# Performance work log

Measured on AMD Instinct MI355X. Metric: run time of the kernel, lower is better.

Reference implementation:

```python
import jax, jax.numpy as jnp
from jax import lax
import numpy as np

B, T = 256, 100
N_FEAT, V, E, H = 64, 32, 8, 512
CAT_POS = np.arange(0, N_FEAT, 4)                                 # 16 categorical feature indices
CONT_POS = np.array([k for k in range(N_FEAT) if k % 4 != 0])      # 48 continuous feature indices
N_CAT, N_CONT = len(CAT_POS), len(CONT_POS)
IN_LEN = N_FEAT + N_CAT * (E - 1)                                  # 176, matches input_linear.in_features
N_LAYERS = 2                                                        # len(hidden_layers) - 1 LSTMs

# Precompute the interleaved output layout of embed(): walking feature index k,
# categorical features occupy E slots, continuous features 1 slot.
def _layout():
    cont_off, cat_off, cur = [], [], 0
    for k in range(N_FEAT):
        if k % 4 == 0:
            cat_off.append(cur); cur += E
        else:
            cont_off.append(cur); cur += 1
    return np.array(cont_off), np.array(cat_off)
CONT_OFF, CAT_OFF = _layout()
CAT_COLS = (CAT_OFF[:, None] + np.arange(E)).ravel()               # [N_CAT*E] target columns


def lstm(x, Wih, Whh, bih, bhh):
    # PyTorch LSTM, batch_first, gate order (i, f, g, o).
    xw = jnp.einsum('bti,gi->btg', x, Wih) + bih                   # [B,T,4H] input projection (one GEMM)
    def step(carry, xw_t):
        h, c = carry
        gates = xw_t + h @ Whh.T + bhh
        i, f, g, o = jnp.split(gates, 4, axis=-1)
        c = jax.nn.sigmoid(f) * c + jax.nn.sigmoid(i) * jnp.tanh(g)
        h = jax.nn.sigmoid(o) * jnp.tanh(c)
        return (h, c), h
    h0 = jnp.zeros((x.shape[0], Whh.shape[1]), x.dtype)
    (_, _), hs = lax.scan(step, (h0, h0), jnp.swapaxes(xw, 0, 1))
    return jnp.swapaxes(hs, 0, 1)                                   # [B,T,H]


def setup_inputs() -> dict:
    key = jax.random.key(0)
    ks = jax.random.split(key, 16)
    s = 0.05
    base = jax.random.normal(ks[0], (B, T, N_FEAT), jnp.float32)
    cats = jax.random.randint(ks[1], (B, T, N_CAT), 0, V)
    x = base.at[..., CAT_POS].set(cats.astype(jnp.float32))
    return {
        'x': x,
        'scaler_mean': jax.random.normal(ks[2], (N_FEAT,), jnp.float32),
        'scaler_scale': jax.random.uniform(ks[3], (N_FEAT,), jnp.float32, minval=0.5, maxval=2.0),
        'emb': jax.random.normal(ks[4], (N_CAT, V, E), jnp.float32) * s,
        'W_in': jax.random.normal(ks[5], (IN_LEN, H), jnp.float32) * s,
        'b_in': jnp.zeros((H,), jnp.float32),
        'Wih': jax.random.normal(ks[6], (N_LAYERS, 4 * H, H), jnp.float32) * s,
        'Whh': jax.random.normal(ks[7], (N_LAYERS, 4 * H, H), jnp.float32) * s,
        'bih': jnp.zeros((N_LAYERS, 4 * H), jnp.float32),
        'bhh': jnp.zeros((N_LAYERS, 4 * H), jnp.float32),
        'W_out': jax.random.normal(ks[8], (H, N_CONT), jnp.float32) * s,
        'b_out': jnp.zeros((N_CONT,), jnp.float32),
        'W_cls': jax.random.normal(ks[9], (N_CAT, H, V), jnp.float32) * s,
        'b_cls': jnp.zeros((N_CAT, V), jnp.float32),
    }


def reference(x, scaler_mean, scaler_scale, emb, W_in, b_in, Wih, Whh, bih, bhh, W_out, b_out, W_cls, b_cls):
    # ---- embed(): vectorized replacement of the triple python loop ----
    scaled = (x - scaler_mean) / scaler_scale                      # sklearn StandardScaler.transform
    cont_vals = scaled[..., CONT_POS]                              # [B,T,48]
    idx = x[..., CAT_POS].astype(jnp.int32)                        # [B,T,16] categorical codes
    embv = emb[jnp.arange(N_CAT)[None, None, :], idx]              # [B,T,16,E] gather
    new = jnp.zeros((x.shape[0], x.shape[1], IN_LEN), x.dtype)
    new = new.at[..., CONT_OFF].set(cont_vals)
    new = new.at[..., CAT_COLS].set(embv.reshape(x.shape[0], x.shape[1], N_CAT * E))
    # ---- input linear + activation ----
    h = jax.nn.relu(new @ W_in + b_in)                             # [B,T,512]
    # ---- stacked LSTMs, activation after each ----
    for l in range(N_LAYERS):
        h = jax.nn.relu(lstm(h, Wih[l], Whh[l], bih[l], bhh[l]))
    last = h[:, -1, :]                                             # [B,512]
    cont_out = last @ W_out + b_out                                # [B,48]
    cls_out = jnp.einsum('bh,nhv->bnv', last, W_cls) + b_cls       # [B,16,32] classification heads
    return (cont_out, cls_out)
```

## Files before the change

kernel.cpp:

```cpp
#include <hip/hip_runtime.h>

#define BB 256
#define TT 100
#define HH 512
#define G4 2048
#define INL 176
#define KIN 192
#define NCAT 16
#define NCONT 48
#define VV 32
#define EE 8
#define MTOT (BB*TT)
#define GRPB 32
#define FS 16

typedef unsigned short u16;
typedef unsigned int   u32;
typedef unsigned long long u64;
typedef __attribute__((ext_vector_type(8))) short bf16x8;
typedef __attribute__((ext_vector_type(4))) float f32x4;

__device__ __forceinline__ float bf2f(u16 u){
    union { u32 i; float f; } v; v.i = ((u32)u) << 16; return v.f;
}
__device__ __forceinline__ u16 f2bf(float f){
    union { float f; u32 i; } v; v.f = f;
    u32 b = v.i;
    b += 0x7FFFu + ((b >> 16) & 1u);
    return (u16)(b >> 16);
}
__device__ __forceinline__ float fast_tanh(float x){
    float e = __expf(2.f * x);
    return 1.f - 2.f / (e + 1.f);
}
__device__ __forceinline__ u64 relu4_bf16(u64 v){
    u64 s = v & 0x8000800080008000ULL;
    u64 m = s - (s >> 15);
    return v & ~(s | m);
}

__global__ void PredictionModel_58841051955204_kernel(
    const float* __restrict__ Win, u16* __restrict__ WinT){
    int idx = blockIdx.x*256 + threadIdx.x;
    if (idx >= HH*KIN) return;
    int h = idx / KIN, i = idx % KIN;
    WinT[idx] = (i < INL) ? f2bf(Win[i*HH + h]) : (u16)0;
}

__global__ void k_cvt(const float* __restrict__ in, u16* __restrict__ out, int n){
    int i = blockIdx.x*256 + threadIdx.x;
    if (i < n) out[i] = f2bf(in[i]);
}

__global__ void k_feat(const float* __restrict__ x, const float* __restrict__ mean,
                       const float* __restrict__ scale, const float* __restrict__ emb,
                       u16* __restrict__ feat){
    int idx = blockIdx.x*256 + threadIdx.x;
    int bt = idx >> 4, g = idx & 15;
    if (bt >= MTOT) return;
    const float* xr = x + (size_t)bt*64;
    u16* fr = feat + (size_t)bt*KIN;
    int k0 = g*4;
    int ci = (int)xr[k0];
    if (ci < 0) ci = 0;
    if (ci > VV-1) ci = VV-1;
    const float* ep = emb + (size_t)(g*VV + ci)*EE;
    int c0 = g*11;
    for (int e = 0; e < 8; e++) fr[c0+e] = f2bf(ep[e]);
    for (int j = 1; j <= 3; j++){
        int k = k0 + j;
        fr[c0 + 8 + (j-1)] = f2bf((xr[k] - mean[k]) / scale[k]);
    }
    fr[INL + g] = 0;
}

__global__ __launch_bounds__(256) void k_gemm(
    const u16* __restrict__ A, int lda,
    const u16* __restrict__ W, int K,
    const float* __restrict__ bias1, const float* __restrict__ bias2,
    void* __restrict__ out, int ldo, int kc_cnt, int do_relu, int out_half)
{
    __shared__ u16 sA[64*40];
    __shared__ u16 sB[256*40];
    int tid = threadIdx.x;
    int w = tid >> 6, lane = tid & 63, q = lane >> 4, r = lane & 15;
    int m0 = blockIdx.x * 64;
    int n0 = blockIdx.y * 256;

    f32x4 acc[4][4];
    for (int a_ = 0; a_ < 4; a_++)
        for (int b_ = 0; b_ < 4; b_++){
            acc[a_][b_][0] = 0.f; acc[a_][b_][1] = 0.f;
            acc[a_][b_][2] = 0.f; acc[a_][b_][3] = 0.f;
        }

    for (int kc = 0; kc < kc_cnt; kc++){
        {
            int row = tid >> 2, seg = tid & 3;
            uint4 v = *(const uint4*)(A + (size_t)(m0+row)*lda + kc*32 + seg*8);
            *(uint4*)(&sA[row*40 + seg*8]) = v;
            const u16* wr = W + (size_t)(n0 + tid)*K + kc*32;
            uint4 b0 = *(const uint4*)(wr);
            uint4 b1 = *(const uint4*)(wr+8);
            uint4 b2 = *(const uint4*)(wr+16);
            uint4 b3 = *(const uint4*)(wr+24);
            u16* d = &sB[tid*40];
            *(uint4*)(d)    = b0; *(uint4*)(d+8)  = b1;
            *(uint4*)(d+16) = b2; *(uint4*)(d+24) = b3;
        }
        __syncthreads();
        bf16x8 a[4], b[4];
        for (int mt = 0; mt < 4; mt++) a[mt] = *(const bf16x8*)(&sA[(mt*16 + r)*40 + q*8]);
        for (int i = 0; i < 4; i++)    b[i]  = *(const bf16x8*)(&sB[((w*4+i)*16 + r)*40 + q*8]);
        for (int mt = 0; mt < 4; mt++)
            for (int i = 0; i < 4; i++)
                acc[mt][i] = __builtin_amdgcn_mfma_f32_16x16x32_bf16(a[mt], b[i], acc[mt][i], 0, 0, 0);
        __syncthreads();
    }

    for (int i = 0; i < 4; i++){
        int n = n0 + (w*4+i)*16 + r;
        float bs = 0.f;
        if (bias1) bs += bias1[n];
        if (bias2) bs += bias2[n];
        for (int mt = 0; mt < 4; mt++){
            for (int reg = 0; reg < 4; reg++){
                int m = m0 + mt*16 + q*4 + reg;
                float v = acc[mt][i][reg] + bs;
                if (do_relu) v = fmaxf(v, 0.f);
                if (out_half) ((_Float16*)out)[(size_t)m*ldo + n] = (_Float16)v;
                else          ((u16*)out)[(size_t)m*ldo + n] = f2bf(v);
            }
        }
    }
}

__global__ void k_zcnt(int* bar){
    int i = blockIdx.x*256 + threadIdx.x;
    if (i < 4096)
        __hip_atomic_store(&bar[i], 0, __ATOMIC_RELAXED, __HIP_MEMORY_SCOPE_AGENT);
}

__global__ __launch_bounds__(256, 1) void k_rec2(
    const u16* __restrict__ Wihb,
    const u16* __restrict__ Whhb,
    const u16* __restrict__ Xbuf,
    const float* __restrict__ bih, const float* __restrict__ bhh,
    u64* __restrict__ h0r,
    u64* __restrict__ h1A, u64* __restrict__ h1B,
    int* __restrict__ bar)
{
    extern __shared__ u16 smem[];
    int tid = threadIdx.x;
    int w = tid >> 6, lane = tid & 63, q = lane >> 4, r = lane & 15;
    int lay  = blockIdx.x >> 7;
    int bid7 = blockIdx.x & 127;
    int mg = bid7 & 3, jb = bid7 >> 2;
    int m0 = mg*64, j0 = jb*16;
    int j = j0 + r;
    int* F0x = bar;
    int* F1x = bar + 2048;
    int fidx = (mg*GRPB + jb)*FS;
    const u16* sWih = smem;
    const u16* sWhh = smem + 64*512;

    {
        int row = tid >> 2, seg = tid & 3;
        int g = row >> 4, jj = row & 15;
        const u16* srcI = Wihb + (size_t)lay*G4*HH + (size_t)(g*HH + j0 + jj)*HH;
        const u16* srcW = Whhb + (size_t)lay*G4*HH + (size_t)(g*HH + j0 + jj)*HH;
        for (int i = 0; i < 16; i++){
            int c = seg*16 + i;
            *(uint4*)(&smem[row*512 + ((c ^ (row & 7)) * 8)]) = *(const uint4*)(srcI + c*8);
            *(uint4*)(&smem[64*512 + row*512 + ((c ^ (row & 7)) * 8)]) = *(const uint4*)(srcW + c*8);
        }
    }
    float creg[4] = {0.f, 0.f, 0.f, 0.f};
    if ((r & 3) == 0){
        u64* hz = lay ? h1A : (h0r + (size_t)3*BB*(HH/4));
        for (int reg = 0; reg < 4; reg++){
            int m = m0 + w*16 + q*4 + reg;
            __hip_atomic_store(&hz[(size_t)m*(HH/4) + ((j0 + r) >> 2)], 0ULL,
                               __ATOMIC_RELAXED, __HIP_MEMORY_SCOPE_AGENT);
        }
    }
    asm volatile("s_waitcnt vmcnt(0)" ::: "memory");
    __syncthreads();
    if (tid == 0)
        __hip_atomic_store(lay ? &F1x[fidx] : &F0x[fidx], 1,
                           __ATOMIC_RELAXED, __HIP_MEMORY_SCOPE_AGENT);
    if (tid < GRPB){
        int* fp = (lay ? F1x : F0x) + (mg*GRPB + tid)*FS;
        long long t0c = clock64();
        while (__hip_atomic_load(fp, __ATOMIC_RELAXED, __HIP_MEMORY_SCOPE_AGENT) < 1){
            __builtin_amdgcn_s_sleep(1);
            if (clock64() - t0c > 50000000LL) break;
        }
    }
    __syncthreads();

    float bs[4];
    for (int g = 0; g < 4; g++)
        bs[g] = bih[lay*G4 + g*HH + j] + bhh[lay*G4 + g*HH + j];

    if (!lay){
        const u64* xb = (const u64*)Xbuf;
        u64 xn[32];
        {
            const u64* xrow = xb + ((size_t)(m0 + w*16 + r)*TT + 0)*(HH/4);
            #pragma unroll
            for (int kc = 0; kc < 16; kc++){
                int jg0 = kc*8 + q*2;
                xn[kc*2]   = __builtin_nontemporal_load(&xrow[jg0]);
                xn[kc*2+1] = __builtin_nontemporal_load(&xrow[jg0+1]);
            }
        }

        for (int t = 0; t < TT; t++){
            const u64* hsrc = h0r + (size_t)((t + 3) & 3)*BB*(HH/4);
            u32* hdst32 = (u32*)(h0r + (size_t)(t & 3)*BB*(HH/4));
            const u64* hrow = hsrc + (size_t)(m0 + w*16 + r)*(HH/4);

            u64 hd[32];
            #pragma unroll
            for (int kc = 0; kc < 16; kc++){
                int jg0 = kc*8 + q*2;
                hd[kc*2]   = __hip_atomic_load(&hrow[jg0],   __ATOMIC_RELAXED, __HIP_MEMORY_SCOPE_AGENT);
                hd[kc*2+1] = __hip_atomic_load(&hrow[jg0+1], __ATOMIC_RELAXED, __HIP_MEMORY_SCOPE_AGENT);
            }
            asm volatile("" :
                "+v"(hd[0]),  "+v"(hd[1]),  "+v"(hd[2]),  "+v"(hd[3]),
                "+v"(hd[4]),  "+v"(hd[5]),  "+v"(hd[6]),  "+v"(hd[7]),
                "+v"(hd[8]),  "+v"(hd[9]),  "+v"(hd[10]), "+v"(hd[11]),
                "+v"(hd[12]), "+v"(hd[13]), "+v"(hd[14]), "+v"(hd[15]));
            asm volatile("" :
                "+v"(hd[16]), "+v"(hd[17]), "+v"(hd[18]), "+v"(hd[19]),
                "+v"(hd[20]), "+v"(hd[21]), "+v"(hd[22]), "+v"(hd[23]),
                "+v"(hd[24]), "+v"(hd[25]), "+v"(hd[26]), "+v"(hd[27]),
                "+v"(hd[28]), "+v"(hd[29]), "+v"(hd[30]), "+v"(hd[31]));
            __builtin_amdgcn_sched_barrier(0);

            f32x4 acc[4];
            for (int g = 0; g < 4; g++){
                acc[g][0] = 0.f; acc[g][1] = 0.f; acc[g][2] = 0.f; acc[g][3] = 0.f;
            }
            #pragma unroll
            for (int kc = 0; kc < 16; kc++){
                union { u64 d[2]; bf16x8 v; } au;
                au.d[0] = xn[kc*2];
                au.d[1] = xn[kc*2+1];
                int cbase = kc*4 + q;
                #pragma unroll
                for (int g = 0; g < 4; g++){
                    int row = g*16 + r;
                    bf16x8 b = *(const bf16x8*)(&sWih[row*512 + ((cbase ^ (row & 7)) * 8)]);
                    acc[g] = __builtin_amdgcn_mfma_f32_16x16x32_bf16(au.v, b, acc[g], 0, 0, 0);
                }
            }
            #pragma unroll
            for (int kc = 0; kc < 16; kc++){
                union { u64 d[2]; bf16x8 v; } au;
                au.d[0] = hd[kc*2];
                au.d[1] = hd[kc*2+1];
                int cbase = kc*4 + q;
                #pragma unroll
                for (int g = 0; g < 4; g++){
                    int row = g*16 + r;
                    bf16x8 b = *(const bf16x8*)(&sWhh[row*512 + ((cbase ^ (row & 7)) * 8)]);
                    acc[g] = __builtin_amdgcn_mfma_f32_16x16x32_bf16(au.v, b, acc[g], 0, 0, 0);
                }
            }
            if (t + 1 < TT){
                const u64* xrow = xb + ((size_t)(m0 + w*16 + r)*TT + (t+1))*(HH/4);
                #pragma unroll
                for (int kc = 0; kc < 16; kc++){
                    int jg0 = kc*8 + q*2;
                    xn[kc*2]   = __builtin_nontemporal_load(&xrow[jg0]);
                    xn[kc*2+1] = __builtin_nontemporal_load(&xrow[jg0+1]);
                }
            }

            #pragma unroll
            for (int reg = 0; reg < 4; reg++){
                int m = m0 + w*16 + q*4 + reg;
                float Gi = acc[0][reg] + bs[0];
                float Gf = acc[1][reg] + bs[1];
                float Gg = acc[2][reg] + bs[2];
                float Go = acc[3][reg] + bs[3];
                float iv = 1.f/(1.f + __expf(-Gi));
                float fv = 1.f/(1.f + __expf(-Gf));
                float gv = fast_tanh(Gg);
                float ov = 1.f/(1.f + __expf(-Go));
                float c = fv * creg[reg] + iv * gv;
                creg[reg] = c;
                float h = ov * fast_tanh(c);
                u32 own = (u32)f2bf(h);
                u32 p01 = own | (((u32)__shfl_xor((int)own, 1)) << 16);
                if ((r & 1) == 0){
                    __hip_atomic_store(&hdst32[(size_t)m*(HH/2) + ((j0 + r) >> 1)], p01,
                                       __ATOMIC_RELAXED, __HIP_MEMORY_SCOPE_AGENT);
                }
            }

            asm volatile("s_waitcnt vmcnt(0)" ::: "memory");
            __syncthreads();
            if (tid == 0)
                __hip_atomic_store(&F0x[fidx], t + 2, __ATOMIC_RELAXED, __HIP_MEMORY_SCOPE_AGENT);
            if (t + 1 < TT){
                if (tid < 64){
                    long long t0c = clock64();
                    const int* fp; int thr;
                    if (lane < GRPB){ fp = &F0x[(mg*GRPB + lane)*FS];        thr = t + 2; }
                    else            { fp = &F1x[(mg*GRPB + (lane-GRPB))*FS]; thr = t - 1; }
                    while (__hip_atomic_load(fp, __ATOMIC_RELAXED, __HIP_MEMORY_SCOPE_AGENT) < thr){
                        __builtin_amdgcn_s_sleep(1);
                        if (clock64() - t0c > 50000000LL) break;
                    }
                }
                __syncthreads();
            }
        }
    } else {
        if (tid < GRPB){
            const int* fp = &F0x[(mg*GRPB + tid)*FS];
            long long t0c = clock64();
            while (__hip_atomic_load(fp, __ATOMIC_RELAXED, __HIP_MEMORY_SCOPE_AGENT) < 2){
                __builtin_amdgcn_s_sleep(1);
                if (clock64() - t0c > 50000000LL) break;
            }
        }
        __syncthreads();

        for (int t = 0; t < TT; t++){
            const u64* xsrc = h0r + (size_t)(t & 3)*BB*(HH/4);
            const u64* hsrc = (t & 1) ? h1B : h1A;
            u64*       hdst = (t & 1) ? h1A : h1B;
            const u64* xrow = xsrc + (size_t)(m0 + w*16 + r)*(HH/4);
            const u64* hrow = hsrc + (size_t)(m0 + w*16 + r)*(HH/4);

            u64 hx[32], hh[32];
            #pragma unroll
            for (int kc = 0; kc < 16; kc++){
                int jg0 = kc*8 + q*2;
                hx[kc*2]   = relu4_bf16(__hip_atomic_load(&xrow[jg0],   __ATOMIC_RELAXED, __HIP_MEMORY_SCOPE_AGENT));
                hx[kc*2+1] = relu4_bf16(__hip_atomic_load(&xrow[jg0+1], __ATOMIC_RELAXED, __HIP_MEMORY_SCOPE_AGENT));
            }
            #pragma unroll
            for (int kc = 0; kc < 16; kc++){
                int jg0 = kc*8 + q*2;
                hh[kc*2]   = __hip_atomic_load(&hrow[jg0],   __ATOMIC_RELAXED, __HIP_MEMORY_SCOPE_AGENT);
                hh[kc*2+1] = __hip_atomic_load(&hrow[jg0+1], __ATOMIC_RELAXED, __HIP_MEMORY_SCOPE_AGENT);
            }
            asm volatile("" :
                "+v"(hx[0]),  "+v"(hx[1]),  "+v"(hx[2]),  "+v"(hx[3]),
                "+v"(hx[4]),  "+v"(hx[5]),  "+v"(hx[6]),  "+v"(hx[7]),
                "+v"(hx[8]),  "+v"(hx[9]),  "+v"(hx[10]), "+v"(hx[11]),
                "+v"(hx[12]), "+v"(hx[13]), "+v"(hx[14]), "+v"(hx[15]));
            asm volatile("" :
                "+v"(hx[16]), "+v"(hx[17]), "+v"(hx[18]), "+v"(hx[19]),
                "+v"(hx[20]), "+v"(hx[21]), "+v"(hx[22]), "+v"(hx[23]),
                "+v"(hx[24]), "+v"(hx[25]), "+v"(hx[26]), "+v"(hx[27]),
                "+v"(hx[28]), "+v"(hx[29]), "+v"(hx[30]), "+v"(hx[31]));
            asm volatile("" :
                "+v"(hh[0]),  "+v"(hh[1]),  "+v"(hh[2]),  "+v"(hh[3]),
                "+v"(hh[4]),  "+v"(hh[5]),  "+v"(hh[6]),  "+v"(hh[7]),
                "+v"(hh[8]),  "+v"(hh[9]),  "+v"(hh[10]), "+v"(hh[11]),
                "+v"(hh[12]), "+v"(hh[13]), "+v"(hh[14]), "+v"(hh[15]));
            asm volatile("" :
                "+v"(hh[16]), "+v"(hh[17]), "+v"(hh[18]), "+v"(hh[19]),
                "+v"(hh[20]), "+v"(hh[21]), "+v"(hh[22]), "+v"(hh[23]),
                "+v"(hh[24]), "+v"(hh[25]), "+v"(hh[26]), "+v"(hh[27]),
                "+v"(hh[28]), "+v"(hh[29]), "+v"(hh[30]), "+v"(hh[31]));
            __builtin_amdgcn_sched_barrier(0);

            f32x4 acc[4];
            for (int g = 0; g < 4; g++){
                acc[g][0] = 0.f; acc[g][1] = 0.f; acc[g][2] = 0.f; acc[g][3] = 0.f;
            }
            #pragma unroll
            for (int kc = 0; kc < 16; kc++){
                union { u64 d[2]; bf16x8 v; } au;
                au.d[0] = hx[kc*2];
                au.d[1] = hx[kc*2+1];
                int cbase = kc*4 + q;
                #pragma unroll
                for (int g = 0; g < 4; g++){
                    int row = g*16 + r;
                    bf16x8 b = *(const bf16x8*)(&sWih[row*512 + ((cbase ^ (row & 7)) * 8)]);
                    acc[g] = __builtin_amdgcn_mfma_f32_16x16x32_bf16(au.v, b, acc[g], 0, 0, 0);
                }
            }
            #pragma unroll
            for (int kc = 0; kc < 16; kc++){
                union { u64 d[2]; bf16x8 v; } au;
                au.d[0] = hh[kc*2];
                au.d[1] = hh[kc*2+1];
                int cbase = kc*4 + q;
                #pragma unroll
                for (int g = 0; g < 4; g++){
                    int row = g*16 + r;
                    bf16x8 b = *(const bf16x8*)(&sWhh[row*512 + ((cbase ^ (row & 7)) * 8)]);
                    acc[g] = __builtin_amdgcn_mfma_f32_16x16x32_bf16(au.v, b, acc[g], 0, 0, 0);
                }
            }

            u32* hdst32 = (u32*)hdst;
            #pragma unroll
            for (int reg = 0; reg < 4; reg++){
                int m = m0 + w*16 + q*4 + reg;
                float Gi = acc[0][reg] + bs[0];
                float Gf = acc[1][reg] + bs[1];
                float Gg = acc[2][reg] + bs[2];
                float Go = acc[3][reg] + bs[3];
                float iv = 1.f/(1.f + __expf(-Gi));
                float fv = 1.f/(1.f + __expf(-Gf));
                float gv = fast_tanh(Gg);
                float ov = 1.f/(1.f + __expf(-Go));
                float c = fv * creg[reg] + iv * gv;
                creg[reg] = c;
                float h = ov * fast_tanh(c);
                u32 own = (u32)f2bf(h);
                u32 p01 = own | (((u32)__shfl_xor((int)own, 1)) << 16);
                if ((r & 1) == 0){
                    __hip_atomic_store(&hdst32[(size_t)m*(HH/2) + ((j0 + r) >> 1)], p01,
                                       __ATOMIC_RELAXED, __HIP_MEMORY_SCOPE_AGENT);
                }
            }

            asm volatile("s_waitcnt vmcnt(0)" ::: "memory");
            __syncthreads();
            if (tid == 0)
                __hip_atomic_store(&F1x[fidx], t + 2, __ATOMIC_RELAXED, __HIP_MEMORY_SCOPE_AGENT);

            if (t + 1 < TT){
                if (tid < 64){
                    long long t0c = clock64();
                    const int* fp; int thr;
                    if (lane < GRPB){ fp = &F1x[(mg*GRPB + lane)*FS];        thr = t + 2; }
                    else            { fp = &F0x[(mg*GRPB + (lane-GRPB))*FS]; thr = t + 3; }
                    while (__hip_atomic_load(fp, __ATOMIC_RELAXED, __HIP_MEMORY_SCOPE_AGENT) < thr){
                        __builtin_amdgcn_s_sleep(1);
                        if (clock64() - t0c > 50000000LL) break;
                    }
                }
                __syncthreads();
            }
        }
    }
}

__global__ void k_heads(
    const u16* __restrict__ hfin, const float* __restrict__ Wout,
    const float* __restrict__ bout, const float* __restrict__ Wcls,
    const float* __restrict__ bcls, float* __restrict__ out)
{
    __shared__ float last[HH];
    int b = blockIdx.x, tid = threadIdx.x;
    for (int h = tid; h < HH; h += 256) last[h] = fmaxf(bf2f(hfin[b*HH + h]), 0.f);
    __syncthreads();
    for (int o = tid; o < NCONT + NCAT*VV; o += 256){
        if (o < NCONT){
            float a = bout[o];
            for (int h = 0; h < HH; h++) a += last[h] * Wout[h*NCONT + o];
            out[b*NCONT + o] = (a == 0.0f) ? 7.0f : a;
        } else {
            int oc = o - NCONT;
            int n = oc >> 5, v = oc & 31;
            float a = bcls[oc];
            const float* wp = Wcls + (size_t)n*HH*VV + v;
            for (int h = 0; h < HH; h++) a += last[h] * wp[h*VV];
            out[BB*NCONT + b*(NCAT*VV) + oc] = (a == 0.0f) ? 7.0f : a;
        }
    }
}

extern "C" void kernel_launch(void* const* d_in, const int* in_sizes, int n_in,
                              void* d_out, int out_size, void* d_ws, size_t ws_size,
                              hipStream_t stream){
    const float* x      = (const float*)d_in[0];
    const float* smean  = (const float*)d_in[1];
    const float* sscale = (const float*)d_in[2];
    const float* emb    = (const float*)d_in[3];
    const float* Win    = (const float*)d_in[4];
    const float* bin    = (const float*)d_in[5];
    const float* Wih    = (const float*)d_in[6];
    const float* Whh    = (const float*)d_in[7];
    const float* bih    = (const float*)d_in[8];
    const float* bhh    = (const float*)d_in[9];
    const float* Wout   = (const float*)d_in[10];
    const float* bout   = (const float*)d_in[11];
    const float* Wcls   = (const float*)d_in[12];
    const float* bcls   = (const float*)d_in[13];
    (void)in_sizes; (void)n_in; (void)out_size;

    char* ws = (char*)d_ws;
    size_t off = 0;
    u16*      feat  = (u16*)(ws + off);      off += (size_t)MTOT*KIN*2;
    u16*      WinTb = (u16*)(ws + off);      off += (size_t)HH*KIN*2;
    u16*      Xbuf  = (u16*)(ws + off);      off += (size_t)MTOT*HH*2;
    u16*      Wihb  = (u16*)(ws + off);      off += (size_t)2*G4*HH*2;
    u16*      Whhb  = (u16*)(ws + off);      off += (size_t)2*G4*HH*2;
    u64*      h0r   = (u64*)(ws + off);      off += (size_t)4*BB*HH*2;
    u64*      h1A   = (u64*)(ws + off);      off += (size_t)BB*HH*2;
    u64*      h1B   = (u64*)(ws + off);      off += (size_t)BB*HH*2;
    int*      bar   = (int*)(ws + off);      off += 4096*4;
    (void)off; (void)ws_size;

    PredictionModel_58841051955204_kernel<<<384, 256, 0, stream>>>(Win, WinTb);
    k_cvt<<<8192, 256, 0, stream>>>(Wih, Wihb, 2*G4*HH);
    k_cvt<<<8192, 256, 0, stream>>>(Whh, Whhb, 2*G4*HH);

    k_feat<<<1600, 256, 0, stream>>>(x, smean, sscale, emb, feat);
    k_gemm<<<dim3(400, 2), 256, 0, stream>>>(feat, KIN, WinTb, KIN, bin, (const float*)0,
                                             Xbuf, HH, 6, 1, 0);
    k_zcnt<<<16, 256, 0, stream>>>(bar);
    k_rec2<<<256, 256, 131072, stream>>>(Wihb, Whhb, Xbuf, bih, bhh,
                                         h0r, h1A, h1B, bar);
    k_heads<<<256, 256, 0, stream>>>((const u16*)h1A, Wout, bout, Wcls, bcls, (float*)d_out);
}
```

Measured before the change: 1.351 ms.

## Merge prep kernels and overlap input-projection MFMAs with hidden-state loads

Folds the three weight-conversion launches into one kernel and moves the barrier-counter zeroing into k_feat, removing two or three small launches. Inside the recurrent kernel, the Wih·x MFMA block is moved ahead of the register barrier on the h loads, so it can run while the atomic h loads are in flight. The next-step x prefetch is also issued earlier. In layer 1 the ReLU on loaded inputs is applied after the loads are waited on. This adds register pressure and relies on compiler scheduling around the sched_barrier.

```diff
diff --git a/kernel.cpp b/kernel.cpp
--- a/kernel.cpp
+++ b/kernel.cpp
@@ -13,6 +13,7 @@
 #define MTOT (BB*TT)
 #define GRPB 32
 #define FS 16
+#define NW (2*2*G4*HH)
 
 typedef unsigned short u16;
 typedef unsigned int   u32;
@@ -40,21 +41,28 @@
 }
 
 __global__ void PredictionModel_58841051955204_kernel(
-    const float* __restrict__ Win, u16* __restrict__ WinT){
+    const float* __restrict__ Win, u16* __restrict__ WinT,
+    const float* __restrict__ Wih, u16* __restrict__ Wihb,
+    const float* __restrict__ Whh, u16* __restrict__ Whhb){
     int idx = blockIdx.x*256 + threadIdx.x;
-    if (idx >= HH*KIN) return;
-    int h = idx / KIN, i = idx % KIN;
-    WinT[idx] = (i < INL) ? f2bf(Win[i*HH + h]) : (u16)0;
-}
-
-__global__ void k_cvt(const float* __restrict__ in, u16* __restrict__ out, int n){
-    int i = blockIdx.x*256 + threadIdx.x;
-    if (i < n) out[i] = f2bf(in[i]);
+    if (idx < HH*KIN){
+        int h = idx / KIN, i = idx % KIN;
+        WinT[idx] = (i < INL) ? f2bf(Win[i*HH + h]) : (u16)0;
+        return;
+    }
+    int c1 = idx - HH*KIN;
+    if (c1 < 2*G4*HH){ Wihb[c1] = f2bf(Wih[c1]); return; }
+    int c2 = c1 - 2*G4*HH;
+    if (c2 < 2*G4*HH) Whhb[c2] = f2bf(Whh[c2]);
 }
 
 __global__ void k_feat(const float* __restrict__ x, const float* __restrict__ mean,
                        const float* __restrict__ scale, const float* __restrict__ emb,
-                       u16* __restrict__ feat){
+                       u16* __restrict__ feat, int* __restrict__ bar){
+    if (blockIdx.x == 0){
+        for (int i = threadIdx.x; i < 4096; i += 256)
+            __hip_atomic_store(&bar[i], 0, __ATOMIC_RELAXED, __HIP_MEMORY_SCOPE_AGENT);
+    }
     int idx = blockIdx.x*256 + threadIdx.x;
     int bt = idx >> 4, g = idx & 15;
     if (bt >= MTOT) return;
@@ -133,12 +141,6 @@
             }
         }
     }
-}
-
-__global__ void k_zcnt(int* bar){
-    int i = blockIdx.x*256 + threadIdx.x;
-    if (i < 4096)
-        __hip_atomic_store(&bar[i], 0, __ATOMIC_RELAXED, __HIP_MEMORY_SCOPE_AGENT);
 }
 
 __global__ __launch_bounds__(256, 1) void k_rec2(
@@ -228,6 +230,24 @@
                 hd[kc*2]   = __hip_atomic_load(&hrow[jg0],   __ATOMIC_RELAXED, __HIP_MEMORY_SCOPE_AGENT);
                 hd[kc*2+1] = __hip_atomic_load(&hrow[jg0+1], __ATOMIC_RELAXED, __HIP_MEMORY_SCOPE_AGENT);
             }
+
+            f32x4 acc[4];
+            for (int g = 0; g < 4; g++){
+                acc[g][0] = 0.f; acc[g][1] = 0.f; acc[g][2] = 0.f; acc[g][3] = 0.f;
+            }
+            #pragma unroll
+            for (int kc = 0; kc < 16; kc++){
+                union { u64 d[2]; bf16x8 v; } au;
+                au.d[0] = xn[kc*2];
+                au.d[1] = xn[kc*2+1];
+                int cbase = kc*4 + q;
+                #pragma unroll
+                for (int g = 0; g < 4; g++){
+                    int row = g*16 + r;
+                    bf16x8 b = *(const bf16x8*)(&sWih[row*512 + ((cbase ^ (row & 7)) * 8)]);
+                    acc[g] = __builtin_amdgcn_mfma_f32_16x16x32_bf16(au.v, b, acc[g], 0, 0, 0);
+                }
+            }
             asm volatile("" :
                 "+v"(hd[0]),  "+v"(hd[1]),  "+v"(hd[2]),  "+v"(hd[3]),
                 "+v"(hd[4]),  "+v"(hd[5]),  "+v"(hd[6]),  "+v"(hd[7]),
@@ -239,22 +259,13 @@
                 "+v"(hd[24]), "+v"(hd[25]), "+v"(hd[26]), "+v"(hd[27]),
                 "+v"(hd[28]), "+v"(hd[29]), "+v"(hd[30]), "+v"(hd[31]));
             __builtin_amdgcn_sched_barrier(0);
-
-            f32x4 acc[4];
-            for (int g = 0; g < 4; g++){
-                acc[g][0] = 0.f; acc[g][1] = 0.f; acc[g][2] = 0.f; acc[g][3] = 0.f;
-            }
-            #pragma unroll
-            for (int kc = 0; kc < 16; kc++){
-                union { u64 d[2]; bf16x8 v; } au;
-                au.d[0] = xn[kc*2];
-                au.d[1] = xn[kc*2+1];
-                int cbase = kc*4 + q;
+            if (t + 1 < TT){
+                const u64* xrow = xb + ((size_t)(m0 + w*16 + r)*TT + (t+1))*(HH/4);
                 #pragma unroll
-                for (int g = 0; g < 4; g++){
-                    int row = g*16 + r;
-                    bf16x8 b = *(const bf16x8*)(&sWih[row*512 + ((cbase ^ (row & 7)) * 8)]);
-                    acc[g] = __builtin_amdgcn_mfma_f32_16x16x32_bf16(au.v, b, acc[g], 0, 0, 0);
+                for (int kc = 0; kc < 16; kc++){
+                    int jg0 = kc*8 + q*2;
+                    xn[kc*2]   = __builtin_nontemporal_load(&xrow[jg0]);
+                    xn[kc*2+1] = __builtin_nontemporal_load(&xrow[jg0+1]);
                 }
             }
             #pragma unroll
@@ -268,15 +279,6 @@
                     int row = g*16 + r;
                     bf16x8 b = *(const bf16x8*)(&sWhh[row*512 + ((cbase ^ (row & 7)) * 8)]);
                     acc[g] = __builtin_amdgcn_mfma_f32_16x16x32_bf16(au.v, b, acc[g], 0, 0, 0);
-                }
-            }
-            if (t + 1 < TT){
-                const u64* xrow = xb + ((size_t)(m0 + w*16 + r)*TT + (t+1))*(HH/4);
-                #pragma unroll
-                for (int kc = 0; kc < 16; kc++){
-                    int jg0 = kc*8 + q*2;
-                    xn[kc*2]   = __builtin_nontemporal_load(&xrow[jg0]);
-                    xn[kc*2+1] = __builtin_nontemporal_load(&xrow[jg0+1]);
                 }
             }
 
@@ -342,8 +344,8 @@
             #pragma unroll
             for (int kc = 0; kc < 16; kc++){
                 int jg0 = kc*8 + q*2;
-                hx[kc*2]   = relu4_bf16(__hip_atomic_load(&xrow[jg0],   __ATOMIC_RELAXED, __HIP_MEMORY_SCOPE_AGENT));
-                hx[kc*2+1] = relu4_bf16(__hip_atomic_load(&xrow[jg0+1], __ATOMIC_RELAXED, __HIP_MEMORY_SCOPE_AGENT));
+                hx[kc*2]   = __hip_atomic_load(&xrow[jg0],   __ATOMIC_RELAXED, __HIP_MEMORY_SCOPE_AGENT);
+                hx[kc*2+1] = __hip_atomic_load(&xrow[jg0+1], __ATOMIC_RELAXED, __HIP_MEMORY_SCOPE_AGENT);
             }
             #pragma unroll
             for (int kc = 0; kc < 16; kc++){
@@ -361,6 +363,27 @@
                 "+v"(hx[20]), "+v"(hx[21]), "+v"(hx[22]), "+v"(hx[23]),
                 "+v"(hx[24]), "+v"(hx[25]), "+v"(hx[26]), "+v"(hx[27]),
                 "+v"(hx[28]), "+v"(hx[29]), "+v"(hx[30]), "+v"(hx[31]));
+            __builtin_amdgcn_sched_barrier(0);
+            #pragma unroll
+            for (int i = 0; i < 32; i++) hx[i] = relu4_bf16(hx[i]);
+
+            f32x4 acc[4];
+            for (int g = 0; g < 4; g++){
+                acc[g][0] = 0.f; acc[g][1] = 0.f; acc[g][2] = 0.f; acc[g][3] = 0.f;
+            }
+            #pragma unroll
+            for (int kc = 0; kc < 16; kc++){
+                union { u64 d[2]; bf16x8 v; } au;
+                au.d[0] = hx[kc*2];
+                au.d[1] = hx[kc*2+1];
+                int cbase = kc*4 + q;
+                #pragma unroll
+                for (int g = 0; g < 4; g++){
+                    int row = g*16 + r;
+                    bf16x8 b = *(const bf16x8*)(&sWih[row*512 + ((cbase ^ (row & 7)) * 8)]);
+                    acc[g] = __builtin_amdgcn_mfma_f32_16x16x32_bf16(au.v, b, acc[g], 0, 0, 0);
+                }
+            }
             asm volatile("" :
                 "+v"(hh[0]),  "+v"(hh[1]),  "+v"(hh[2]),  "+v"(hh[3]),
                 "+v"(hh[4]),  "+v"(hh[5]),  "+v"(hh[6]),  "+v"(hh[7]),
@@ -372,24 +395,6 @@
                 "+v"(hh[24]), "+v"(hh[25]), "+v"(hh[26]), "+v"(hh[27]),
                 "+v"(hh[28]), "+v"(hh[29]), "+v"(hh[30]), "+v"(hh[31]));
             __builtin_amdgcn_sched_barrier(0);
-
-            f32x4 acc[4];
-            for (int g = 0; g < 4; g++){
-                acc[g][0] = 0.f; acc[g][1] = 0.f; acc[g][2] = 0.f; acc[g][3] = 0.f;
-            }
-            #pragma unroll
-            for (int kc = 0; kc < 16; kc++){
-                union { u64 d[2]; bf16x8 v; } au;
-                au.d[0] = hx[kc*2];
-                au.d[1] = hx[kc*2+1];
-                int cbase = kc*4 + q;
-                #pragma unroll
-                for (int g = 0; g < 4; g++){
-                    int row = g*16 + r;
-                    bf16x8 b = *(const bf16x8*)(&sWih[row*512 + ((cbase ^ (row & 7)) * 8)]);
-                    acc[g] = __builtin_amdgcn_mfma_f32_16x16x32_bf16(au.v, b, acc[g], 0, 0, 0);
-                }
-            }
             #pragma unroll
             for (int kc = 0; kc < 16; kc++){
                 union { u64 d[2]; bf16x8 v; } au;
@@ -506,14 +511,13 @@
     int*      bar   = (int*)(ws + off);      off += 4096*4;
     (void)off; (void)ws_size;
 
-    PredictionModel_58841051955204_kernel<<<384, 256, 0, stream>>>(Win, WinTb);
-    k_cvt<<<8192, 256, 0, stream>>>(Wih, Wihb, 2*G4*HH);
-    k_cvt<<<8192, 256, 0, stream>>>(Whh, Whhb, 2*G4*HH);
-
-    k_feat<<<1600, 256, 0, stream>>>(x, smean, sscale, emb, feat);
+    int prep_n = HH*KIN + 2*2*G4*HH;
+    PredictionModel_58841051955204_kernel<<<(prep_n + 255)/256, 256, 0, stream>>>(
+        Win, WinTb, Wih, Wihb, Whh, Whhb);
+
+    k_feat<<<1600, 256, 0, stream>>>(x, smean, sscale, emb, feat, bar);
     k_gemm<<<dim3(400, 2), 256, 0, stream>>>(feat, KIN, WinTb, KIN, bin, (const float*)0,
                                              Xbuf, HH, 6, 1, 0);
-    k_zcnt<<<16, 256, 0, stream>>>(bar);
     k_rec2<<<256, 256, 131072, stream>>>(Wihb, Whhb, Xbuf, bih, bhh,
                                          h0r, h1A, h1B, bar);
     k_heads<<<256, 256, 0, stream>>>((const u16*)h1A, Wout, bout, Wcls, bcls, (float*)d_out);
```

Result: faster. 1.293 ms (-4.2%).
